# Optimization experiments

Hardware: AMD Instinct MI355X
Metric: run time of the kernel (lower is better)

Reference implementation:

```python
import jax, jax.numpy as jnp
import numpy as np

B, E, IN, OUT = 512, 8, 1024, 1024


def setup_inputs() -> dict:
    key = jax.random.key(0)
    k1, k2, k3, k4 = jax.random.split(key, 4)
    x = jax.random.normal(k1, (B, IN), dtype=jnp.float32)
    expert_weights = jax.random.uniform(k2, (B, E), dtype=jnp.float32)
    # kaiming_uniform per expert with a=sqrt(5): bound = sqrt(6/((1+a^2)*fan_in)) = 1/sqrt(fan_in)
    wb = 1.0 / np.sqrt(IN)
    weight = jax.random.uniform(k3, (E, OUT, IN), dtype=jnp.float32, minval=-wb, maxval=wb)
    bias = jax.random.uniform(k4, (E, OUT), dtype=jnp.float32, minval=-wb, maxval=wb)
    return {"x": x, "expert_weights": expert_weights, "weight": weight, "bias": bias}


def reference(x, expert_weights, weight, bias):
    # Same math as: blended_W = einsum('bk,koi->boi'); bmm(blended_W, x[...,None]) + blended_b
    # fused as a single contraction to avoid the [B, out, in] intermediate.
    y = jnp.einsum('bk,koi,bi->bo', expert_weights, weight, x)
    b = jnp.einsum('bk,ko->bo', expert_weights, bias)
    return y + b
```

## Files before the change

### kernel.cpp

```cpp
#include <hip/hip_runtime.h>
#include <hip/hip_bf16.h>


#define EDIM 8
#define INDIM 1024
#define OUTDIM 1024
#define BATCH 512
#define TM 128
#define TNR 64
#define BK 64
#define NITER (INDIM / BK)

typedef __attribute__((ext_vector_type(8))) short frag8;
typedef __attribute__((ext_vector_type(4))) float f32x4;

__device__ inline void async_ld16(void* lds, const void* g) {
  __builtin_amdgcn_global_load_lds(
      (const __attribute__((address_space(1))) void*)g,
      (__attribute__((address_space(3))) void*)lds, 16, 0, 0);
}

__device__ inline ushort f2bf(float f) {
  unsigned u = __builtin_bit_cast(unsigned, f);
  u += 0x7fffu + ((u >> 16) & 1u);
  return (ushort)(u >> 16);
}

__device__ inline ushort4 f4_to_bf4(float4 v) {
  ushort4 o;
  o.x = f2bf(v.x); o.y = f2bf(v.y); o.z = f2bf(v.z); o.w = f2bf(v.w);
  return o;
}

__global__ __launch_bounds__(256) void prep_x(const float* __restrict__ x,
                                              ushort* __restrict__ wsX) {
  int i = blockIdx.x * 256 + threadIdx.x;
  ((ushort4*)wsX)[i] = f4_to_bf4(((const float4*)x)[i]);
}

__global__ __launch_bounds__(256, 2) void gemm_fused(
    const ushort* __restrict__ Xb,
    const float* __restrict__ ew,
    const float* __restrict__ W,
    const float* __restrict__ bias,
    float* __restrict__ out) {
  __shared__ __align__(16) ushort As[2 * TM * BK];
  __shared__ __align__(16) ushort Bs[2 * TNR * BK];

  const int tid  = threadIdx.x;
  const int lane = tid & 63;
  const int wave = tid >> 6;
  const int o0 = blockIdx.x * 8;
  const int m0 = blockIdx.y * TM;

  const int l15  = lane & 15;
  const int quad = lane >> 4;

  const int arow   = lane >> 3;
  const int akslot = (lane & 7) ^ arow;
  const ushort* aG = Xb + (size_t)(m0 + arow) * INDIM + akslot * 8;

  const float* bG[4];
  int bWoff[4];
#pragma unroll
  for (int p = 0; p < 4; ++p) {
    int fi = tid + 256 * p;
    int rb = fi >> 4, gs = fi & 15;
    bG[p] = W + (size_t)((rb >> 3) * 1024 + o0 + (rb & 7)) * INDIM + gs * 4;
    bWoff[p] = rb * 64 + (((gs >> 1) ^ (rb & 7)) * 8) + (gs & 1) * 4;
  }

  f32x4 acc[2][4] = {};

#pragma unroll
  for (int cc = 0; cc < 4; ++cc) {
    int c = wave * 4 + cc;
    async_ld16(&As[c * 512], aG + (size_t)c * 8 * INDIM);
  }
#pragma unroll
  for (int p = 0; p < 4; ++p)
    *(ushort4*)&Bs[bWoff[p]] = f4_to_bf4(*(const float4*)bG[p]);
  __syncthreads();

  for (int it = 0; it < NITER; ++it) {
    const int cur = it & 1, nxt = cur ^ 1;
    const bool more = (it + 1 < NITER);
    float4 bv[4];
    if (more) {
      const int kn = (it + 1) * BK;
#pragma unroll
      for (int cc = 0; cc < 4; ++cc) {
        int c = wave * 4 + cc;
        async_ld16(&As[nxt * (TM * BK) + c * 512],
                   aG + (size_t)c * 8 * INDIM + kn);
      }
#pragma unroll
      for (int p = 0; p < 4; ++p) bv[p] = *(const float4*)(bG[p] + kn);
    }

#pragma unroll
    for (int kk8 = 0; kk8 < 8; kk8 += 4) {
      frag8 a[2], b[4];
#pragma unroll
      for (int i = 0; i < 2; ++i) {
        int ra = wave * 32 + i * 16 + l15;
        a[i] = *(const frag8*)&As[cur * (TM * BK) + ra * 64 +
                                  (((quad + kk8) ^ (ra & 7)) * 8)];
      }
#pragma unroll
      for (int j = 0; j < 4; ++j) {
        int rb = j * 16 + l15;
        b[j] = *(const frag8*)&Bs[cur * (TNR * BK) + rb * 64 +
                                  (((quad + kk8) ^ (rb & 7)) * 8)];
      }
#pragma unroll
      for (int i = 0; i < 2; ++i)
#pragma unroll
        for (int j = 0; j < 4; ++j)
          acc[i][j] = __builtin_amdgcn_mfma_f32_16x16x32_bf16(a[i], b[j], acc[i][j], 0, 0, 0);
    }

    if (more) {
#pragma unroll
      for (int p = 0; p < 4; ++p)
        *(ushort4*)&Bs[nxt * (TNR * BK) + bWoff[p]] = f4_to_bf4(bv[p]);
    }
    __syncthreads();
  }

  const int h  = l15 >> 3;
  const int oc = o0 + (l15 & 7);
  float bg[4];
#pragma unroll
  for (int j = 0; j < 4; ++j) bg[j] = bias[(2 * j + h) * OUTDIM + oc];

#pragma unroll
  for (int i = 0; i < 2; ++i) {
#pragma unroll
    for (int r = 0; r < 4; ++r) {
      const int b = m0 + wave * 32 + i * 16 + quad * 4 + r;
      float p = 0.f;
#pragma unroll
      for (int j = 0; j < 4; ++j)
        p += ew[b * EDIM + 2 * j + h] * (acc[i][j][r] + bg[j]);
      p += __shfl_xor(p, 8, 64);
      if (h == 0) out[(size_t)b * OUTDIM + oc] = p;
    }
  }
}

__global__ __launch_bounds__(256) void fallback_kernel(
    const float* __restrict__ x, const float* __restrict__ ew,
    const float* __restrict__ W, const float* __restrict__ bias,
    float* __restrict__ out) {
  int idx = blockIdx.x * 256 + threadIdx.x;
  int b = idx >> 10;
  int o = idx & 1023;
  float y = 0.f;
  for (int k = 0; k < EDIM; ++k) {
    const float* wr = W + ((size_t)k * OUTDIM + o) * INDIM;
    const float* xr = x + (size_t)b * INDIM;
    float dot = 0.f;
    for (int i = 0; i < INDIM; ++i) dot += wr[i] * xr[i];
    y += ew[b * EDIM + k] * (dot + bias[k * OUTDIM + o]);
  }
  out[idx] = y;
}

extern "C" void kernel_launch(void* const* d_in, const int* in_sizes, int n_in,
                              void* d_out, int out_size, void* d_ws, size_t ws_size,
                              hipStream_t stream) {
  const float* x    = (const float*)d_in[0];
  const float* ew   = (const float*)d_in[1];
  const float* W    = (const float*)d_in[2];
  const float* bias = (const float*)d_in[3];
  float* out = (float*)d_out;

  if (ws_size < (size_t)(BATCH * INDIM * 2)) {
    fallback_kernel<<<2048, 256, 0, stream>>>(x, ew, W, bias, out);
    return;
  }
  ushort* wsX = (ushort*)d_ws;

  prep_x<<<512, 256, 0, stream>>>(x, wsX);
  gemm_fused<<<dim3(OUTDIM / 8, BATCH / TM), 256, 0, stream>>>(
      wsX, ew, W, bias, out);
}
```

Before: 99.84 us.

## Fuse x conversion and GEMM into one cooperative kernel with grid sync

Merges the bf16 conversion of x and the fused expert GEMM into a single cooperative kernel. Each block converts a slice of x, all blocks meet at a grid-wide barrier, and then the GEMM runs as before. The goal is to drop one kernel launch and the gap between the two kernels. The cost is a grid-wide sync, which needs all 512 blocks to be co-resident; if the cooperative launch fails, the code falls back to the old two-kernel path.

```diff
diff --git a/kernel.cpp b/kernel.cpp
--- a/kernel.cpp
+++ b/kernel.cpp
@@ -1,5 +1,6 @@
 #include <hip/hip_runtime.h>
 #include <hip/hip_bf16.h>
+#include <hip/hip_cooperative_groups.h>
 
 
 #define EDIM 8
@@ -32,21 +33,12 @@
   return o;
 }
 
-__global__ __launch_bounds__(256) void prep_x(const float* __restrict__ x,
-                                              ushort* __restrict__ wsX) {
-  int i = blockIdx.x * 256 + threadIdx.x;
-  ((ushort4*)wsX)[i] = f4_to_bf4(((const float4*)x)[i]);
-}
-
-__global__ __launch_bounds__(256, 2) void gemm_fused(
-    const ushort* __restrict__ Xb,
-    const float* __restrict__ ew,
-    const float* __restrict__ W,
-    const float* __restrict__ bias,
-    float* __restrict__ out) {
-  __shared__ __align__(16) ushort As[2 * TM * BK];
-  __shared__ __align__(16) ushort Bs[2 * TNR * BK];
-
+__device__ void gemm_body(const ushort* __restrict__ Xb,
+                          const float* __restrict__ ew,
+                          const float* __restrict__ W,
+                          const float* __restrict__ bias,
+                          float* __restrict__ out,
+                          ushort* As, ushort* Bs) {
   const int tid  = threadIdx.x;
   const int lane = tid & 63;
   const int wave = tid >> 6;
@@ -58,7 +50,7 @@
 
   const int arow   = lane >> 3;
   const int akslot = (lane & 7) ^ arow;
-  const ushort* aG = Xb + (size_t)(m0 + arow) * INDIM + akslot * 8;
+  const ushort* aG = Xb + (size_t)((m0 + arow)) * INDIM + akslot * 8;
 
   const float* bG[4];
   int bWoff[4];
@@ -147,6 +139,37 @@
       if (h == 0) out[(size_t)b * OUTDIM + oc] = p;
     }
   }
+}
+
+__global__ __launch_bounds__(256, 2) void fused_coop(
+    const float* __restrict__ x, const float* __restrict__ ew,
+    const float* __restrict__ W, const float* __restrict__ bias,
+    float* __restrict__ out, ushort* __restrict__ wsX) {
+  __shared__ __align__(16) ushort As[2 * TM * BK];
+  __shared__ __align__(16) ushort Bs[2 * TNR * BK];
+
+  {
+    int i = (blockIdx.y * gridDim.x + blockIdx.x) * 256 + threadIdx.x;
+    ((ushort4*)wsX)[i] = f4_to_bf4(((const float4*)x)[i]);
+  }
+  cooperative_groups::this_grid().sync();
+
+  gemm_body(wsX, ew, W, bias, out, As, Bs);
+}
+
+__global__ __launch_bounds__(256) void prep_x(const float* __restrict__ x,
+                                              ushort* __restrict__ wsX) {
+  int i = blockIdx.x * 256 + threadIdx.x;
+  ((ushort4*)wsX)[i] = f4_to_bf4(((const float4*)x)[i]);
+}
+
+__global__ __launch_bounds__(256, 2) void gemm_fused(
+    const ushort* __restrict__ Xb, const float* __restrict__ ew,
+    const float* __restrict__ W, const float* __restrict__ bias,
+    float* __restrict__ out) {
+  __shared__ __align__(16) ushort As[2 * TM * BK];
+  __shared__ __align__(16) ushort Bs[2 * TNR * BK];
+  gemm_body(Xb, ew, W, bias, out, As, Bs);
 }
 
 __global__ __launch_bounds__(256) void fallback_kernel(
@@ -182,7 +205,14 @@
   }
   ushort* wsX = (ushort*)d_ws;
 
-  prep_x<<<512, 256, 0, stream>>>(x, wsX);
-  gemm_fused<<<dim3(OUTDIM / 8, BATCH / TM), 256, 0, stream>>>(
-      wsX, ew, W, bias, out);
-}
+  void* args[] = {(void*)&x, (void*)&ew, (void*)&W, (void*)&bias,
+                  (void*)&out, (void*)&wsX};
+  hipError_t rc = hipLaunchCooperativeKernel(
+      (const void*)fused_coop, dim3(OUTDIM / 8, BATCH / TM), dim3(256),
+      args, 0, stream);
+  if (rc != hipSuccess) {
+    prep_x<<<512, 256, 0, stream>>>(x, wsX);
+    gemm_fused<<<dim3(OUTDIM / 8, BATCH / TM), 256, 0, stream>>>(
+        wsX, ew, W, bias, out);
+  }
+}
```

Result: slower. 149.6 us (+49.9%).
